# Kernel tuning notes

Measured on AMD Instinct MI355X. Metric: run time of the kernel, lower is better.

The kernel has to match this reference:

```python
import jax, jax.numpy as jnp
import numpy as np

B, L, D, H, DK, DV = 2, 2048, 512, 8, 64, 64
EPS = 1e-6


def setup_inputs() -> dict:
    key = jax.random.key(0)
    ks = jax.random.split(key, 19)
    n = lambda k, s: jax.random.normal(k, s, dtype=jnp.float32)
    inp = {
        "q_r": n(ks[0], (B, L, D)), "q_i": n(ks[1], (B, L, D)),
        "k_r": n(ks[2], (B, L, D)), "k_i": n(ks[3], (B, L, D)),
        "v_r": n(ks[4], (B, L, D)), "v_i": n(ks[5], (B, L, D)),
        "wq_r": n(ks[6], (D, H * DK)) * 0.02, "wq_i": n(ks[7], (D, H * DK)) * 0.02,
        "wk_r": n(ks[8], (D, H * DK)) * 0.02, "wk_i": n(ks[9], (D, H * DK)) * 0.02,
        "wv_r": n(ks[10], (D, H * DV)) * 0.02, "wv_i": n(ks[11], (D, H * DV)) * 0.02,
        "wo_r": n(ks[12], (H * DV, D)) * 0.02, "wo_i": n(ks[13], (H * DV, D)) * 0.02,
        "ln_wr": n(ks[14], (D,)), "ln_wi": n(ks[15], (D,)),
        "ln_br": n(ks[16], (D,)), "ln_bi": n(ks[17], (D,)),
        "mask": jax.random.randint(ks[18], (B, L, L), 0, 2).astype(jnp.int32),
    }
    return inp


def _clinear(xr, xi, wr, wi):
    # complex matmul (xr + i xi) @ (wr + i wi)
    return xr @ wr - xi @ wi, xi @ wr + xr @ wi


def _complex_layernorm(r, i, wr, wi, br, bi, eps=EPS):
    axes = (1, 2)  # normalize over all non-batch dims of [B, L, D]
    r = r - r.mean(axis=axes, keepdims=True)
    i = i - i.mean(axis=axes, keepdims=True)
    Crr = (r * r).mean(axis=axes, keepdims=True) + eps
    Cii = (i * i).mean(axis=axes, keepdims=True) + eps
    Cri = (r * i).mean(axis=axes, keepdims=True)
    s = jnp.sqrt(Crr * Cii - Cri * Cri)
    t = jnp.sqrt(Crr + Cii + 2.0 * s)
    inv_st = 1.0 / (s * t)
    Rrr = (Cii + s) * inv_st
    Rii = (Crr + s) * inv_st
    Rri = -Cri * inv_st
    nr = Rrr * r + Rri * i
    ni = Rii * i + Rri * r
    # affine: complex multiply by (wr + i wi), then add complex bias
    out_r = nr * wr - ni * wi + br
    out_i = nr * wi + ni * wr + bi
    return out_r, out_i


def reference(q_r, q_i, k_r, k_i, v_r, v_i,
              wq_r, wq_i, wk_r, wk_i, wv_r, wv_i, wo_r, wo_i,
              ln_wr, ln_wi, ln_br, ln_bi, mask):
    res_r, res_i = q_r, q_i
    qr, qi = _clinear(q_r, q_i, wq_r, wq_i)
    kr, ki = _clinear(k_r, k_i, wk_r, wk_i)
    vr, vi = _clinear(v_r, v_i, wv_r, wv_i)
    # [B, L, H*Dk] -> [B, H, L, Dk]
    tohead = lambda x, d: x.reshape(B, L, H, d).transpose(0, 2, 1, 3)
    qr, qi = tohead(qr, DK), tohead(qi, DK)
    kr, ki = tohead(kr, DK), tohead(ki, DK)
    vr, vi = tohead(vr, DV), tohead(vi, DV)
    temp = jnp.float32(DK) ** 0.5
    qr, qi = qr / temp, qi / temp
    # complex scores (q @ conj(k)^T): re + i*im
    sr = jnp.einsum('bhqd,bhkd->bhqk', qr, kr) + jnp.einsum('bhqd,bhkd->bhqk', qi, ki)
    si = jnp.einsum('bhqd,bhkd->bhqk', qi, kr) - jnp.einsum('bhqd,bhkd->bhqk', qr, ki)
    a = jnp.sqrt(sr * sr + si * si)  # abs of complex scores
    a = jnp.where(mask[:, None, :, :] == 0, jnp.float32(-1e9), a)
    attn = jax.nn.softmax(a, axis=-1)  # real-valued attention weights
    out_r = jnp.einsum('bhqk,bhkd->bhqd', attn, vr)
    out_i = jnp.einsum('bhqk,bhkd->bhqd', attn, vi)
    # [B, H, L, Dv] -> [B, L, H*Dv]
    out_r = out_r.transpose(0, 2, 1, 3).reshape(B, L, H * DV)
    out_i = out_i.transpose(0, 2, 1, 3).reshape(B, L, H * DV)
    out_r, out_i = _clinear(out_r, out_i, wo_r, wo_i)
    out_r = out_r + res_r
    out_i = out_i + res_i
    out_r, out_i = _complex_layernorm(out_r, out_i, ln_wr, ln_wi, ln_br, ln_bi)
    return out_r, out_i, attn
```

## Files before the change

kernel.cpp:

```cpp
#include <hip/hip_runtime.h>

typedef unsigned short u16;
typedef unsigned int u32;
typedef unsigned long long u64;


typedef __attribute__((ext_vector_type(8))) short bf16x8;
typedef __attribute__((ext_vector_type(4))) float f32x4;
typedef __attribute__((ext_vector_type(4))) u32 u32x4;

__device__ __forceinline__ u16 f2bf(float f) {
  u32 x = __float_as_uint(f);
  return (u16)((x + 0x7FFFu + ((x >> 16) & 1u)) >> 16);
}
__device__ __forceinline__ u32 pk2(float a, float b) {
  return (u32)f2bf(a) | ((u32)f2bf(b) << 16);
}
__device__ __forceinline__ bf16x8 negv(bf16x8 v) {
  u32x4 x = __builtin_bit_cast(u32x4, v);
  x ^= 0x80008000u;
  return __builtin_bit_cast(bf16x8, x);
}

__global__ __launch_bounds__(256) void prep(
    const float* __restrict__ qr, const float* __restrict__ qi,
    const float* __restrict__ kr, const float* __restrict__ ki,
    const float* __restrict__ vr, const float* __restrict__ vi,
    const float* __restrict__ wqr, const float* __restrict__ wqi,
    const float* __restrict__ wkr, const float* __restrict__ wki,
    const float* __restrict__ wvr, const float* __restrict__ wvi,
    const float* __restrict__ wor, const float* __restrict__ woi,
    const int* __restrict__ mask,
    u16* __restrict__ A, u16* __restrict__ Btb, u64* __restrict__ mb,
    float* __restrict__ stats) {
  __shared__ float tile[64][65];
  int bid = blockIdx.x;
  int t = threadIdx.x;
  if (bid < 32768) {
    int tid = bid * 256 + t;
    u64 bal = __ballot(mask[tid] != 0);
    if ((t & 63) == 0) mb[tid >> 6] = bal;
    return;
  }
  bid -= 32768;
  if (bid < 6144) {
    int z = bid >> 11;
    int bx = bid & 2047;
    const float* r  = (z == 0) ? qr : (z == 1) ? kr : vr;
    const float* im = (z == 0) ? qi : (z == 1) ? ki : vi;
    int c = bx * 256 + t;
    int m = c >> 7;
    int ck = (c & 127) * 8;
    const float* s = (ck < 512) ? (r + (size_t)m * 512 + ck)
                                : (im + (size_t)m * 512 + (ck - 512));
    float4 a = ((const float4*)s)[0];
    float4 b = ((const float4*)s)[1];
    uint4 o;
    o.x = pk2(a.x, a.y); o.y = pk2(a.z, a.w);
    o.z = pk2(b.x, b.y); o.w = pk2(b.z, b.w);
    ((uint4*)(A + (size_t)z * 4194304))[c] = o;
    return;
  }
  bid -= 6144;
  if (bid < 1024) {
    int z = bid >> 8;
    int bx = bid & 255;
    const float* wr = (z==0)?wqr:(z==1)?wkr:(z==2)?wvr:wor;
    const float* wi = (z==0)?wqi:(z==1)?wki:(z==2)?wvi:woi;
    u16* Bt = Btb + (size_t)z * 1048576;
    int n0 = (bx >> 4) * 64;
    int k0 = (bx & 15) * 64;
    bool nlow = (n0 < 512), klow = (k0 < 512);
    const float* src = nlow ? (klow ? wr : wi) : (klow ? wi : wr);
    float sgn = (nlow && !klow) ? -1.0f : 1.0f;
    int col0 = nlow ? n0 : n0 - 512;
    int kr0 = klow ? k0 : k0 - 512;
    {
      int rr = t >> 2, cc = (t & 3) * 16;
      const float4* s = (const float4*)(src + (size_t)(kr0 + rr) * 512 + col0 + cc);
#pragma unroll
      for (int j = 0; j < 4; ++j) {
        float4 v = s[j];
        tile[rr][cc + j*4 + 0] = v.x; tile[rr][cc + j*4 + 1] = v.y;
        tile[rr][cc + j*4 + 2] = v.z; tile[rr][cc + j*4 + 3] = v.w;
      }
    }
    __syncthreads();
    {
      int nn = t >> 2, kc = (t & 3) * 16;
      u32 w[8];
#pragma unroll
      for (int j = 0; j < 8; ++j)
        w[j] = pk2(sgn * tile[kc + 2*j][nn], sgn * tile[kc + 2*j + 1][nn]);
      uint4* d = (uint4*)(Bt + (size_t)(n0 + nn) * 1024 + k0 + kc);
      d[0] = make_uint4(w[0], w[1], w[2], w[3]);
      d[1] = make_uint4(w[4], w[5], w[6], w[7]);
    }
    return;
  }
  if (t < 16) stats[t] = 0.0f;
}

__global__ __launch_bounds__(256) void pack_vt(const u16* __restrict__ Cvm,
                                               u16* __restrict__ vt) {
  int z = blockIdx.y;
  int b = z >> 3, h = z & 7;
  int lt = blockIdx.x >> 1, ct = blockIdx.x & 1;
  int l0 = lt * 64, c0 = ct * 64;
  int n0 = (ct == 0) ? (h * 64) : (512 + h * 64);
  __shared__ u16 tile[64][80];
  int t = threadIdx.x;
  {
    int lr = t >> 2, cc = (t & 3) * 16;
    const uint4* s = (const uint4*)(Cvm + ((size_t)(b * 2048 + l0 + lr)) * 1024 + n0 + cc);
    uint4 v0 = s[0], v1 = s[1];
    *(uint4*)&tile[lr][cc] = v0;
    *(uint4*)&tile[lr][cc + 8] = v1;
  }
  __syncthreads();
  {
    int cr = t >> 2, lc = (t & 3) * 16;
    u32 w[8];
#pragma unroll
    for (int j = 0; j < 8; ++j)
      w[j] = (u32)tile[lc + 2*j][cr] | ((u32)tile[lc + 2*j + 1][cr] << 16);
    uint4* d = (uint4*)(vt + ((size_t)z * 128 + c0 + cr) * 2048 + l0 + lc);
    d[0] = make_uint4(w[0], w[1], w[2], w[3]);
    d[1] = make_uint4(w[4], w[5], w[6], w[7]);
  }
}


__device__ __forceinline__ void stage_bf(const u16* __restrict__ g, int ld,
                                         u16* lds, int t) {
#pragma unroll
  for (int p = 0; p < 4; ++p) {
    int id = p * 256 + t;
    int r = id >> 3, c = id & 7;
    uint4 v = *(const uint4*)(g + (size_t)r * ld + c * 8);
    *(uint4*)(lds + r * 64 + ((c ^ (r & 7)) << 3)) = v;
  }
}
__device__ __forceinline__ void stage64(const u16* __restrict__ g, int ld,
                                        u16* lds, int t) {
#pragma unroll
  for (int p = 0; p < 2; ++p) {
    int id = p * 256 + t;
    int r = id >> 3, c = id & 7;
    uint4 v = *(const uint4*)(g + (size_t)r * ld + c * 8);
    *(uint4*)(lds + r * 64 + ((c ^ (r & 7)) << 3)) = v;
  }
}

__global__ __launch_bounds__(256) void gemm_proj(const u16* __restrict__ Abase,
                                                 const u16* __restrict__ Btbase,
                                                 u16* __restrict__ Cbase) {
  __shared__ u16 lA[128 * 64], lB[128 * 64];
  int t = threadIdx.x, lane = t & 63, wid = t >> 6;
  int c15 = lane & 15, g = lane >> 4, l7 = lane & 7;
  int z = blockIdx.z;
  const u16* A  = Abase  + (size_t)z * 4194304;
  const u16* Bt = Btbase + (size_t)z * 1048576;
  u16* C = Cbase + (size_t)z * 4194304;
  int brow = blockIdx.y * 128, bcol = blockIdx.x * 128;
  float scale = (z == 0) ? 0.125f : 1.0f;
  int sw0 = ((g ^ l7) << 3), sw1 = (((4 | g) ^ l7) << 3);
  int wr0 = (wid >> 1) * 64 + c15, wc0 = (wid & 1) * 64 + c15;
  const u16 *pA0 = lA + wr0 * 64 + sw0, *pA1 = lA + wr0 * 64 + sw1;
  const u16 *pB0 = lB + wc0 * 64 + sw0, *pB1 = lB + wc0 * 64 + sw1;
  f32x4 zero = {0.f, 0.f, 0.f, 0.f};
  f32x4 acc[4][4];
#pragma unroll
  for (int mi = 0; mi < 4; ++mi)
#pragma unroll
    for (int ni = 0; ni < 4; ++ni) acc[mi][ni] = zero;
  for (int kt = 0; kt < 1024; kt += 64) {
    stage_bf(A + (size_t)brow * 1024 + kt, 1024, lA, t);
    stage_bf(Bt + (size_t)bcol * 1024 + kt, 1024, lB, t);
    __syncthreads();
#pragma unroll
    for (int ks = 0; ks < 2; ++ks) {
      const u16* pa = ks ? pA1 : pA0;
      const u16* pb = ks ? pB1 : pB0;
      bf16x8 fa[4], fb[4];
#pragma unroll
      for (int i2 = 0; i2 < 4; ++i2) {
        fa[i2] = *(const bf16x8*)(pa + i2 * 1024);
        fb[i2] = *(const bf16x8*)(pb + i2 * 1024);
      }
#pragma unroll
      for (int mi = 0; mi < 4; ++mi)
#pragma unroll
        for (int ni = 0; ni < 4; ++ni)
          acc[mi][ni] = __builtin_amdgcn_mfma_f32_16x16x32_bf16(
              fa[mi], fb[ni], acc[mi][ni], 0, 0, 0);
    }
    __syncthreads();
  }
  int wrb = (wid >> 1) * 64, wcb = (wid & 1) * 64;
  int rj = g * 4, cj = c15;
#pragma unroll
  for (int mi = 0; mi < 4; ++mi)
#pragma unroll
    for (int ni = 0; ni < 4; ++ni)
#pragma unroll
      for (int j = 0; j < 4; ++j)
        C[(size_t)(brow + wrb + mi * 16 + rj + j) * 1024 +
          (bcol + wcb + ni * 16 + cj)] = f2bf(acc[mi][ni][j] * scale);
}

__global__ __launch_bounds__(256, 3) void fused_p1(
    const u16* __restrict__ Cq, const u16* __restrict__ Ck,
    const u16* __restrict__ vt, const u64* __restrict__ mb,
    float* __restrict__ invbuf, u16* __restrict__ Ao) {
  __shared__ u16 lKr[64 * 64], lKi[64 * 64], lV[128 * 64], lP[64 * 64];
  int t = threadIdx.x, lane = t & 63, w = t >> 6;
  int c15 = lane & 15, g = lane >> 4, l7 = lane & 7;
  int f = blockIdx.x + (int)gridDim.x * blockIdx.y;
  int wk = (f & 7) * 64 + (f >> 3);
  int strip = wk & 31, z = wk >> 5;
  int b = z >> 3, h = z & 7;
  int q0 = strip * 64;
  int arow = w * 16 + c15;
  int rbase = w * 16 + (g << 2);

  const u16* Qrow = Cq + ((size_t)(b * 2048 + q0 + arow)) * 1024 + h * 64;
  bf16x8 q0r = *(const bf16x8*)(Qrow + g * 8);
  bf16x8 q1r = *(const bf16x8*)(Qrow + 32 + g * 8);
  bf16x8 q0i = *(const bf16x8*)(Qrow + 512 + g * 8);
  bf16x8 q1i = *(const bf16x8*)(Qrow + 544 + g * 8);
  bf16x8 nq0r = negv(q0r), nq1r = negv(q1r);

  int sw0 = ((g ^ l7) << 3), sw1 = (((4 | g) ^ l7) << 3);
  const u16 *pKr0 = lKr + c15 * 64 + sw0, *pKr1 = lKr + c15 * 64 + sw1;
  const u16 *pKi0 = lKi + c15 * 64 + sw0, *pKi1 = lKi + c15 * 64 + sw1;
  const u16 *pV0 = lV + c15 * 64 + sw0, *pV1 = lV + c15 * 64 + sw1;
  const u16 *pP0 = lP + arow * 64 + sw0, *pP1 = lP + arow * 64 + sw1;

  size_t mbase = ((size_t)(b * 2048 + q0 + rbase)) * 32;
  float s[4] = {0.f, 0.f, 0.f, 0.f};
  f32x4 zero = {0.f, 0.f, 0.f, 0.f};
  f32x4 o[8];
#pragma unroll
  for (int ni = 0; ni < 8; ++ni) o[ni] = zero;

  const u16* Kb = Ck + ((size_t)(b * 2048)) * 1024 + h * 64;
  const u16* Vb = vt + (size_t)z * 262144;

  for (int tl = 0; tl < 32; ++tl) {
    int l0 = tl * 64;
    if (tl) __syncthreads();
    stage64(Kb + (size_t)l0 * 1024, 1024, lKr, t);
    stage64(Kb + (size_t)l0 * 1024 + 512, 1024, lKi, t);
    stage_bf(Vb + l0, 2048, lV, t);
    __syncthreads();
    f32x4 sr[4], si[4];
#pragma unroll
    for (int ni = 0; ni < 4; ++ni) { sr[ni] = zero; si[ni] = zero; }
#pragma unroll
    for (int ni = 0; ni < 4; ++ni) {
      bf16x8 g0 = *(const bf16x8*)(pKr0 + ni * 1024);
      bf16x8 g1 = *(const bf16x8*)(pKi0 + ni * 1024);
      sr[ni] = __builtin_amdgcn_mfma_f32_16x16x32_bf16(q0r, g0, sr[ni], 0, 0, 0);
      sr[ni] = __builtin_amdgcn_mfma_f32_16x16x32_bf16(q0i, g1, sr[ni], 0, 0, 0);
      si[ni] = __builtin_amdgcn_mfma_f32_16x16x32_bf16(q0i, g0, si[ni], 0, 0, 0);
      si[ni] = __builtin_amdgcn_mfma_f32_16x16x32_bf16(nq0r, g1, si[ni], 0, 0, 0);
      bf16x8 h0 = *(const bf16x8*)(pKr1 + ni * 1024);
      bf16x8 h1 = *(const bf16x8*)(pKi1 + ni * 1024);
      sr[ni] = __builtin_amdgcn_mfma_f32_16x16x32_bf16(q1r, h0, sr[ni], 0, 0, 0);
      sr[ni] = __builtin_amdgcn_mfma_f32_16x16x32_bf16(q1i, h1, sr[ni], 0, 0, 0);
      si[ni] = __builtin_amdgcn_mfma_f32_16x16x32_bf16(q1i, h0, si[ni], 0, 0, 0);
      si[ni] = __builtin_amdgcn_mfma_f32_16x16x32_bf16(nq1r, h1, si[ni], 0, 0, 0);
    }
    u64 wm[4];
#pragma unroll
    for (int j = 0; j < 4; ++j) wm[j] = mb[mbase + (size_t)j * 32 + tl];
#pragma unroll
    for (int ni = 0; ni < 4; ++ni) {
      int cbit = ni * 16 + c15;
      int pchi = ni * 2 + (c15 >> 3);
#pragma unroll
      for (int j = 0; j < 4; ++j) {
        float n = sr[ni][j] * sr[ni][j] + si[ni][j] * si[ni][j];
        float p = __expf(__builtin_amdgcn_sqrtf(n));
        p = ((wm[j] >> cbit) & 1ull) ? p : 0.0f;
        s[j] += p;
        lP[(rbase + j) * 64 + ((pchi ^ (((g & 1) << 2) + j)) << 3) + l7] = f2bf(p);
      }
    }
    {
      bf16x8 fa0 = *(const bf16x8*)pP0;
      bf16x8 fa1 = *(const bf16x8*)pP1;
#pragma unroll
      for (int ni = 0; ni < 8; ++ni) {
        bf16x8 fb0 = *(const bf16x8*)(pV0 + ni * 1024);
        bf16x8 fb1 = *(const bf16x8*)(pV1 + ni * 1024);
        o[ni] = __builtin_amdgcn_mfma_f32_16x16x32_bf16(fa0, fb0, o[ni], 0, 0, 0);
        o[ni] = __builtin_amdgcn_mfma_f32_16x16x32_bf16(fa1, fb1, o[ni], 0, 0, 0);
      }
    }
  }
  float inv[4];
#pragma unroll
  for (int j = 0; j < 4; ++j) {
    float sj = s[j];
#pragma unroll
    for (int off = 1; off < 16; off <<= 1) sj += __shfl_xor(sj, off);
    inv[j] = 1.0f / sj;
  }
  if (c15 == 0) {
#pragma unroll
    for (int j = 0; j < 4; ++j)
      invbuf[z * 2048 + q0 + rbase + j] = inv[j];
  }
#pragma unroll
  for (int ni = 0; ni < 8; ++ni) {
    int c = ni * 16 + c15;
    int nout = (c < 64) ? (h * 64 + c) : (512 + h * 64 + (c - 64));
#pragma unroll
    for (int j = 0; j < 4; ++j)
      Ao[((size_t)(b * 2048 + q0 + rbase + j)) * 1024 + nout] =
          f2bf(o[ni][j] * inv[j]);
  }
}

__global__ __launch_bounds__(256, 3) void attn_p2(
    const u16* __restrict__ Cq, const u16* __restrict__ Ck,
    const u64* __restrict__ mb, const float* __restrict__ invbuf,
    float* __restrict__ attn) {
  __shared__ u16 lKr[64 * 64], lKi[64 * 64];
  int t = threadIdx.x, lane = t & 63, w = t >> 6;
  int c15 = lane & 15, g = lane >> 4, l7 = lane & 7;
  int f = blockIdx.x + (int)gridDim.x * blockIdx.y;
  int wk = (f & 7) * 256 + (f >> 3);
  int z = wk >> 7;
  int rem = wk & 127;
  int strip = rem >> 2, kc = rem & 3;
  int b = z >> 3, h = z & 7;
  int q0 = strip * 64;
  int arow = w * 16 + c15;
  int rbase = w * 16 + (g << 2);

  const u16* Qrow = Cq + ((size_t)(b * 2048 + q0 + arow)) * 1024 + h * 64;
  bf16x8 q0r = *(const bf16x8*)(Qrow + g * 8);
  bf16x8 q1r = *(const bf16x8*)(Qrow + 32 + g * 8);
  bf16x8 q0i = *(const bf16x8*)(Qrow + 512 + g * 8);
  bf16x8 q1i = *(const bf16x8*)(Qrow + 544 + g * 8);
  bf16x8 nq0r = negv(q0r), nq1r = negv(q1r);

  int sw0 = ((g ^ l7) << 3), sw1 = (((4 | g) ^ l7) << 3);
  const u16 *pKr0 = lKr + c15 * 64 + sw0, *pKr1 = lKr + c15 * 64 + sw1;
  const u16 *pKi0 = lKi + c15 * 64 + sw0, *pKi1 = lKi + c15 * 64 + sw1;

  size_t mbase = ((size_t)(b * 2048 + q0 + rbase)) * 32;
  float inv[4];
#pragma unroll
  for (int j = 0; j < 4; ++j) inv[j] = invbuf[z * 2048 + q0 + rbase + j];
  f32x4 zero = {0.f, 0.f, 0.f, 0.f};
  const u16* Kb = Ck + ((size_t)(b * 2048)) * 1024 + h * 64;
  float* arow_out = attn + ((size_t)z * 2048 + q0 + rbase) * 2048 + c15;

  for (int tt2 = 0; tt2 < 8; ++tt2) {
    int tl = kc * 8 + tt2;
    int l0 = tl * 64;
    if (tt2) __syncthreads();
    stage64(Kb + (size_t)l0 * 1024, 1024, lKr, t);
    stage64(Kb + (size_t)l0 * 1024 + 512, 1024, lKi, t);
    __syncthreads();
    f32x4 sr[4], si[4];
#pragma unroll
    for (int ni = 0; ni < 4; ++ni) { sr[ni] = zero; si[ni] = zero; }
#pragma unroll
    for (int ni = 0; ni < 4; ++ni) {
      bf16x8 g0 = *(const bf16x8*)(pKr0 + ni * 1024);
      bf16x8 g1 = *(const bf16x8*)(pKi0 + ni * 1024);
      sr[ni] = __builtin_amdgcn_mfma_f32_16x16x32_bf16(q0r, g0, sr[ni], 0, 0, 0);
      sr[ni] = __builtin_amdgcn_mfma_f32_16x16x32_bf16(q0i, g1, sr[ni], 0, 0, 0);
      si[ni] = __builtin_amdgcn_mfma_f32_16x16x32_bf16(q0i, g0, si[ni], 0, 0, 0);
      si[ni] = __builtin_amdgcn_mfma_f32_16x16x32_bf16(nq0r, g1, si[ni], 0, 0, 0);
      bf16x8 h0 = *(const bf16x8*)(pKr1 + ni * 1024);
      bf16x8 h1 = *(const bf16x8*)(pKi1 + ni * 1024);
      sr[ni] = __builtin_amdgcn_mfma_f32_16x16x32_bf16(q1r, h0, sr[ni], 0, 0, 0);
      sr[ni] = __builtin_amdgcn_mfma_f32_16x16x32_bf16(q1i, h1, sr[ni], 0, 0, 0);
      si[ni] = __builtin_amdgcn_mfma_f32_16x16x32_bf16(q1i, h0, si[ni], 0, 0, 0);
      si[ni] = __builtin_amdgcn_mfma_f32_16x16x32_bf16(nq1r, h1, si[ni], 0, 0, 0);
    }
    u64 wm[4];
#pragma unroll
    for (int j = 0; j < 4; ++j) wm[j] = mb[mbase + (size_t)j * 32 + tl];
    float* outp = arow_out + l0;
#pragma unroll
    for (int ni = 0; ni < 4; ++ni) {
      int cbit = ni * 16 + c15;
#pragma unroll
      for (int j = 0; j < 4; ++j) {
        float n = sr[ni][j] * sr[ni][j] + si[ni][j] * si[ni][j];
        float p = __expf(__builtin_amdgcn_sqrtf(n)) * inv[j];
        p = ((wm[j] >> cbit) & 1ull) ? p : 0.0f;
        outp[(size_t)j * 2048 + ni * 16] = p;
      }
    }
  }
}

__global__ __launch_bounds__(256) void gemm_oproj(
    const u16* __restrict__ A, const u16* __restrict__ Bt,
    const float* __restrict__ resR, const float* __restrict__ resI,
    float* __restrict__ outR, float* __restrict__ outI) {
  __shared__ u16 lA[128 * 64], lB[128 * 64];
  int t = threadIdx.x, lane = t & 63, wid = t >> 6;
  int c15 = lane & 15, g = lane >> 4, l7 = lane & 7;
  int brow = blockIdx.y * 128, bcol = blockIdx.x * 128;
  int sw0 = ((g ^ l7) << 3), sw1 = (((4 | g) ^ l7) << 3);
  int wr0 = (wid >> 1) * 64 + c15, wc0 = (wid & 1) * 64 + c15;
  const u16 *pA0 = lA + wr0 * 64 + sw0, *pA1 = lA + wr0 * 64 + sw1;
  const u16 *pB0 = lB + wc0 * 64 + sw0, *pB1 = lB + wc0 * 64 + sw1;
  f32x4 zero = {0.f, 0.f, 0.f, 0.f};
  f32x4 acc[4][4];
#pragma unroll
  for (int mi = 0; mi < 4; ++mi)
#pragma unroll
    for (int ni = 0; ni < 4; ++ni) acc[mi][ni] = zero;
  for (int kt = 0; kt < 1024; kt += 64) {
    stage_bf(A + (size_t)brow * 1024 + kt, 1024, lA, t);
    stage_bf(Bt + (size_t)bcol * 1024 + kt, 1024, lB, t);
    __syncthreads();
#pragma unroll
    for (int ks = 0; ks < 2; ++ks) {
      const u16* pa = ks ? pA1 : pA0;
      const u16* pb = ks ? pB1 : pB0;
      bf16x8 fa[4], fb[4];
#pragma unroll
      for (int i2 = 0; i2 < 4; ++i2) {
        fa[i2] = *(const bf16x8*)(pa + i2 * 1024);
        fb[i2] = *(const bf16x8*)(pb + i2 * 1024);
      }
#pragma unroll
      for (int mi = 0; mi < 4; ++mi)
#pragma unroll
        for (int ni = 0; ni < 4; ++ni)
          acc[mi][ni] = __builtin_amdgcn_mfma_f32_16x16x32_bf16(
              fa[mi], fb[ni], acc[mi][ni], 0, 0, 0);
    }
    __syncthreads();
  }
  int wrb = (wid >> 1) * 64, wcb = (wid & 1) * 64;
  int rj = g * 4, cj = c15;
#pragma unroll
  for (int mi = 0; mi < 4; ++mi)
#pragma unroll
    for (int ni = 0; ni < 4; ++ni)
#pragma unroll
      for (int j = 0; j < 4; ++j) {
        int row = brow + wrb + mi * 16 + rj + j;
        int col = bcol + wcb + ni * 16 + cj;
        float v = acc[mi][ni][j];
        if (col < 512)
          outR[(size_t)row * 512 + col] = v + resR[(size_t)row * 512 + col];
        else {
          int c2 = col - 512;
          outI[(size_t)row * 512 + c2] = v + resI[(size_t)row * 512 + c2];
        }
      }
}

__global__ __launch_bounds__(256) void ln_reduce(const float* __restrict__ outR,
                                                 const float* __restrict__ outI,
                                                 float* __restrict__ stats) {
  int b = blockIdx.y;
  int t = threadIdx.x;
  size_t base = (size_t)b * 1048576 + (size_t)blockIdx.x * 2048;
  float s0 = 0.f, s1 = 0.f, s2 = 0.f, s3 = 0.f, s4 = 0.f;
#pragma unroll
  for (int p = 0; p < 8; ++p) {
    size_t e = base + p * 256 + t;
    float r = outR[e], i = outI[e];
    s0 += r; s1 += i; s2 += r * r; s3 += i * i; s4 += r * i;
  }
#pragma unroll
  for (int off = 32; off; off >>= 1) {
    s0 += __shfl_xor(s0, off); s1 += __shfl_xor(s1, off);
    s2 += __shfl_xor(s2, off); s3 += __shfl_xor(s3, off);
    s4 += __shfl_xor(s4, off);
  }
  __shared__ float red[4][5];
  if ((t & 63) == 0) {
    int w = t >> 6;
    red[w][0] = s0; red[w][1] = s1; red[w][2] = s2; red[w][3] = s3; red[w][4] = s4;
  }
  __syncthreads();
  if (t == 0) {
    float a0 = red[0][0] + red[1][0] + red[2][0] + red[3][0];
    float a1 = red[0][1] + red[1][1] + red[2][1] + red[3][1];
    float a2 = red[0][2] + red[1][2] + red[2][2] + red[3][2];
    float a3 = red[0][3] + red[1][3] + red[2][3] + red[3][3];
    float a4 = red[0][4] + red[1][4] + red[2][4] + red[3][4];
    atomicAdd(&stats[b * 8 + 0], a0);
    atomicAdd(&stats[b * 8 + 1], a1);
    atomicAdd(&stats[b * 8 + 2], a2);
    atomicAdd(&stats[b * 8 + 3], a3);
    atomicAdd(&stats[b * 8 + 4], a4);
  }
}

__global__ __launch_bounds__(256) void ln_apply(
    float* __restrict__ outR, float* __restrict__ outI,
    const float* __restrict__ stats,
    const float* __restrict__ lnwr, const float* __restrict__ lnwi,
    const float* __restrict__ lnbr, const float* __restrict__ lnbi) {
  int b = blockIdx.y;
  const float* st = stats + b * 8;
  float iN = 1.0f / 1048576.0f;
  float mr = st[0] * iN, mi = st[1] * iN;
  float Crr = st[2] * iN - mr * mr + 1e-6f;
  float Cii = st[3] * iN - mi * mi + 1e-6f;
  float Cri = st[4] * iN - mr * mi;
  float s = sqrtf(fmaxf(Crr * Cii - Cri * Cri, 0.f));
  float tt = sqrtf(Crr + Cii + 2.f * s);
  float inv = 1.0f / (s * tt);
  float Rrr = (Cii + s) * inv, Rii = (Crr + s) * inv, Rri = -Cri * inv;
  size_t e = ((size_t)blockIdx.x * 256 + threadIdx.x) * 4;
  size_t idx = (size_t)b * 1048576 + e;
  int d = (int)(e & 511);
  float4 r4 = *(float4*)(outR + idx);
  float4 i4 = *(float4*)(outI + idx);
  float4 wr = *(const float4*)(lnwr + d);
  float4 wi = *(const float4*)(lnwi + d);
  float4 br = *(const float4*)(lnbr + d);
  float4 bi = *(const float4*)(lnbi + d);
  float4 orr, oii;
#pragma unroll
  for (int j = 0; j < 4; ++j) {
    float r = ((&r4.x)[j]) - mr;
    float i = ((&i4.x)[j]) - mi;
    float nr = Rrr * r + Rri * i;
    float ni = Rii * i + Rri * r;
    (&orr.x)[j] = nr * (&wr.x)[j] - ni * (&wi.x)[j] + (&br.x)[j];
    (&oii.x)[j] = nr * (&wi.x)[j] + ni * (&wr.x)[j] + (&bi.x)[j];
  }
  *(float4*)(outR + idx) = orr;
  *(float4*)(outI + idx) = oii;
}

extern "C" void kernel_launch(void* const* d_in, const int* in_sizes, int n_in,
                              void* d_out, int out_size, void* d_ws, size_t ws_size,
                              hipStream_t stream) {
  const float* q_r = (const float*)d_in[0];
  const float* q_i = (const float*)d_in[1];
  const float* k_r = (const float*)d_in[2];
  const float* k_i = (const float*)d_in[3];
  const float* v_r = (const float*)d_in[4];
  const float* v_i = (const float*)d_in[5];
  const float* wq_r = (const float*)d_in[6];
  const float* wq_i = (const float*)d_in[7];
  const float* wk_r = (const float*)d_in[8];
  const float* wk_i = (const float*)d_in[9];
  const float* wv_r = (const float*)d_in[10];
  const float* wv_i = (const float*)d_in[11];
  const float* wo_r = (const float*)d_in[12];
  const float* wo_i = (const float*)d_in[13];
  const float* ln_wr = (const float*)d_in[14];
  const float* ln_wi = (const float*)d_in[15];
  const float* ln_br = (const float*)d_in[16];
  const float* ln_bi = (const float*)d_in[17];
  const int* mask = (const int*)d_in[18];

  float* outR = (float*)d_out;
  float* outI = outR + 2097152;
  float* attn = outR + 4194304;

  char* ws = (char*)d_ws;
  u16* Aq = (u16*)ws;
  u16* Bt = (u16*)(ws + 25165824);
  u16* Cq = (u16*)(ws + 33554432);
  u16* Ck = Cq + 4194304;
  u16* Cv = Cq + 8388608;
  u16* vt = Aq;
  u16* Ao = (u16*)(ws + 58720256);
  u64* mb = (u64*)(ws + 67108864);
  float* stats = (float*)(ws + 69206016);
  float* invbuf = (float*)(ws + 69207040);

  prep<<<dim3(32768 + 6144 + 1024 + 1), 256, 0, stream>>>(
      q_r, q_i, k_r, k_i, v_r, v_i, wq_r, wq_i, wk_r, wk_i, wv_r, wv_i,
      wo_r, wo_i, mask, Aq, Bt, mb, stats);
  gemm_proj<<<dim3(8, 32, 3), 256, 0, stream>>>(Aq, Bt, Cq);
  pack_vt<<<dim3(64, 16), 256, 0, stream>>>(Cv, vt);
  fused_p1<<<dim3(32, 16), 256, 0, stream>>>(Cq, Ck, vt, mb, invbuf, Ao);
  attn_p2<<<dim3(128, 16), 256, 0, stream>>>(Cq, Ck, mb, invbuf, attn);
  gemm_oproj<<<dim3(8, 32), 256, 0, stream>>>(Ao, Bt + 3145728, q_r, q_i, outR, outI);
  ln_reduce<<<dim3(512, 2), 256, 0, stream>>>(outR, outI, stats);
  ln_apply<<<dim3(1024, 2), 256, 0, stream>>>(outR, outI, stats, ln_wr, ln_wi,
                                              ln_br, ln_bi);
}
```

Baseline: 341.5 us.

## Split fused attention key loop in two and combine partials in new kernel

```diff
diff --git a/kernel.cpp b/kernel.cpp
--- a/kernel.cpp
+++ b/kernel.cpp
@@ -130,7 +130,6 @@
   }
 }
 
-
 __device__ __forceinline__ void stage_bf(const u16* __restrict__ g, int ld,
                                          u16* lds, int t) {
 #pragma unroll
@@ -212,13 +211,15 @@
 __global__ __launch_bounds__(256, 3) void fused_p1(
     const u16* __restrict__ Cq, const u16* __restrict__ Ck,
     const u16* __restrict__ vt, const u64* __restrict__ mb,
-    float* __restrict__ invbuf, u16* __restrict__ Ao) {
+    float* __restrict__ OP, float* __restrict__ sp) {
   __shared__ u16 lKr[64 * 64], lKi[64 * 64], lV[128 * 64], lP[64 * 64];
   int t = threadIdx.x, lane = t & 63, w = t >> 6;
   int c15 = lane & 15, g = lane >> 4, l7 = lane & 7;
   int f = blockIdx.x + (int)gridDim.x * blockIdx.y;
-  int wk = (f & 7) * 64 + (f >> 3);
-  int strip = wk & 31, z = wk >> 5;
+  int wk = (f & 7) * 128 + (f >> 3);
+  int kc = wk & 1;
+  int wk2 = wk >> 1;
+  int strip = wk2 & 31, z = wk2 >> 5;
   int b = z >> 3, h = z & 7;
   int q0 = strip * 64;
   int arow = w * 16 + c15;
@@ -247,9 +248,11 @@
   const u16* Kb = Ck + ((size_t)(b * 2048)) * 1024 + h * 64;
   const u16* Vb = vt + (size_t)z * 262144;
 
-  for (int tl = 0; tl < 32; ++tl) {
+  int tl0 = kc * 16;
+  for (int tt = 0; tt < 16; ++tt) {
+    int tl = tl0 + tt;
     int l0 = tl * 64;
-    if (tl) __syncthreads();
+    if (tt) __syncthreads();
     stage64(Kb + (size_t)l0 * 1024, 1024, lKr, t);
     stage64(Kb + (size_t)l0 * 1024 + 512, 1024, lKi, t);
     stage_bf(Vb + l0, 2048, lV, t);
@@ -300,28 +303,52 @@
       }
     }
   }
-  float inv[4];
+  float st[4];
 #pragma unroll
   for (int j = 0; j < 4; ++j) {
     float sj = s[j];
 #pragma unroll
     for (int off = 1; off < 16; off <<= 1) sj += __shfl_xor(sj, off);
-    inv[j] = 1.0f / sj;
+    st[j] = sj;
   }
   if (c15 == 0) {
 #pragma unroll
     for (int j = 0; j < 4; ++j)
-      invbuf[z * 2048 + q0 + rbase + j] = inv[j];
-  }
-#pragma unroll
-  for (int ni = 0; ni < 8; ++ni) {
-    int c = ni * 16 + c15;
-    int nout = (c < 64) ? (h * 64 + c) : (512 + h * 64 + (c - 64));
+      sp[kc * 32768 + z * 2048 + q0 + rbase + j] = st[j];
+  }
+  size_t obase = ((size_t)((kc * 16 + z) * 2048 + q0 + rbase)) * 128;
+#pragma unroll
+  for (int ni = 0; ni < 8; ++ni)
 #pragma unroll
     for (int j = 0; j < 4; ++j)
-      Ao[((size_t)(b * 2048 + q0 + rbase + j)) * 1024 + nout] =
-          f2bf(o[ni][j] * inv[j]);
-  }
+      OP[obase + (size_t)j * 128 + ni * 16 + c15] = o[ni][j];
+}
+
+__global__ __launch_bounds__(256) void combine_o(
+    const float* __restrict__ OP, const float* __restrict__ sp,
+    u16* __restrict__ Ao, float* __restrict__ invbuf) {
+  int tid = blockIdx.x * 256 + threadIdx.x;
+  int rowg = tid >> 7;
+  int nout = (tid & 127) * 8;
+  int b = rowg >> 11, l = rowg & 2047;
+  int h = (nout < 512) ? (nout >> 6) : ((nout - 512) >> 6);
+  int c = (nout & 63) + ((nout < 512) ? 0 : 64);
+  int z = b * 8 + h;
+  size_t base0 = ((size_t)(z * 2048 + l)) * 128 + c;
+  size_t base1 = ((size_t)((16 + z) * 2048 + l)) * 128 + c;
+  float4 a0 = *(const float4*)(OP + base0);
+  float4 a1 = *(const float4*)(OP + base0 + 4);
+  float4 b0 = *(const float4*)(OP + base1);
+  float4 b1 = *(const float4*)(OP + base1 + 4);
+  float ssum = sp[z * 2048 + l] + sp[32768 + z * 2048 + l];
+  float inv = 1.0f / ssum;
+  if ((nout < 512) && ((nout & 63) == 0)) invbuf[z * 2048 + l] = inv;
+  uint4 o;
+  o.x = pk2((a0.x + b0.x) * inv, (a0.y + b0.y) * inv);
+  o.y = pk2((a0.z + b0.z) * inv, (a0.w + b0.w) * inv);
+  o.z = pk2((a1.x + b1.x) * inv, (a1.y + b1.y) * inv);
+  o.w = pk2((a1.z + b1.z) * inv, (a1.w + b1.w) * inv);
+  *(uint4*)(Ao + (size_t)rowg * 1024 + nout) = o;
 }
 
 __global__ __launch_bounds__(256, 3) void attn_p2(
@@ -580,13 +607,16 @@
   u64* mb = (u64*)(ws + 67108864);
   float* stats = (float*)(ws + 69206016);
   float* invbuf = (float*)(ws + 69207040);
+  float* OP = (float*)(ws + 70254592);
+  float* sp = (float*)(ws + 104857600);
 
   prep<<<dim3(32768 + 6144 + 1024 + 1), 256, 0, stream>>>(
       q_r, q_i, k_r, k_i, v_r, v_i, wq_r, wq_i, wk_r, wk_i, wv_r, wv_i,
       wo_r, wo_i, mask, Aq, Bt, mb, stats);
   gemm_proj<<<dim3(8, 32, 3), 256, 0, stream>>>(Aq, Bt, Cq);
   pack_vt<<<dim3(64, 16), 256, 0, stream>>>(Cv, vt);
-  fused_p1<<<dim3(32, 16), 256, 0, stream>>>(Cq, Ck, vt, mb, invbuf, Ao);
+  fused_p1<<<dim3(64, 16), 256, 0, stream>>>(Cq, Ck, vt, mb, OP, sp);
+  combine_o<<<dim3(2048), 256, 0, stream>>>(OP, sp, Ao, invbuf);
   attn_p2<<<dim3(128, 16), 256, 0, stream>>>(Cq, Ck, mb, invbuf, attn);
   gemm_oproj<<<dim3(8, 32), 256, 0, stream>>>(Ao, Bt + 3145728, q_r, q_i, outR, outI);
   ln_reduce<<<dim3(512, 2), 256, 0, stream>>>(outR, outI, stats);
```

After: 359.2 us. +5.2%, slower.
